# Kernel tuning notes

Measured on AMD Instinct MI355X. Metric: run time of the kernel, lower is better.

The kernel has to match this reference:

```python
import jax, jax.numpy as jnp
import numpy as np

B, T, N = 128, 1024, 64


def setup_inputs() -> dict:
    key = jax.random.key(0)
    k1, k2, k3, k4, k5 = jax.random.split(key, 5)
    potentials = jax.random.normal(k1, (B, T, N), dtype=jnp.float32)
    tags = jax.random.randint(k2, (B, T), 0, N, dtype=jnp.int32)
    # valid lengths in [T//2, T] so every sequence has at least one step
    sequence_length = jax.random.randint(k3, (B,), T // 2, T + 1, dtype=jnp.int32)
    chain_kernel = jax.random.normal(k4, (N, N), dtype=jnp.float32)
    sample_weight = jax.random.uniform(k5, (B,), dtype=jnp.float32)
    return {
        "potentials": potentials,
        "tags": tags,
        "sequence_length": sequence_length,
        "chain_kernel": chain_kernel,
        "sample_weight": sample_weight,
    }


def _crf_sequence_score(potentials, tags, sequence_length, chain_kernel):
    # potentials: [B,T,N], tags: [B,T] int, chain_kernel: [N,N]
    Bx, Tx, Nx = potentials.shape
    t_idx = jnp.arange(Tx)
    mask = (t_idx[None, :] < sequence_length[:, None]).astype(potentials.dtype)  # [B,T]
    # unary score: potentials at the gold tag per step
    unary = jnp.take_along_axis(potentials, tags[..., None].astype(jnp.int32), axis=2)[..., 0]  # [B,T]
    unary_score = jnp.sum(unary * mask, axis=1)  # [B]
    # binary score: transitions tag[t] -> tag[t+1], valid if t+1 < seq_len
    trans_sc = chain_kernel[tags[:, :-1], tags[:, 1:]]  # [B,T-1]
    binary_score = jnp.sum(trans_sc * mask[:, 1:], axis=1)  # [B]
    return unary_score + binary_score


def _crf_log_norm(potentials, sequence_length, chain_kernel):
    # forward algorithm with lax.scan over time
    Bx, Tx, Nx = potentials.shape
    alpha0 = potentials[:, 0]  # [B,N]
    pots_rest = jnp.transpose(potentials[:, 1:], (1, 0, 2))  # [T-1,B,N]
    step_mask = (jnp.arange(1, Tx)[:, None] < sequence_length[None, :])  # [T-1,B]

    def step(alpha, inp):
        pot_t, m_t = inp  # [B,N], [B]
        # logsumexp over previous tag: alpha[b,i] + trans[i,j]
        new = jax.nn.logsumexp(alpha[:, :, None] + chain_kernel[None], axis=1) + pot_t
        alpha = jnp.where(m_t[:, None], new, alpha)
        return alpha, None

    alpha_T, _ = jax.lax.scan(step, alpha0, (pots_rest, step_mask))
    return jax.nn.logsumexp(alpha_T, axis=1)  # [B]


def reference(potentials, tags, sequence_length, chain_kernel, sample_weight):
    seq_score = _crf_sequence_score(potentials, tags, sequence_length, chain_kernel)
    log_norm = _crf_log_norm(potentials, sequence_length, chain_kernel)
    log_likelihood = seq_score - log_norm  # [B]
    crf_loss = -log_likelihood * sample_weight
    return jnp.mean(crf_loss)
```

## Files before the change

kernel.cpp:

```cpp
#include <hip/hip_runtime.h>
#include <math.h>

#define BB 128
#define TT 1024
#define NN 64
#define NCH 16
#define SCH 64

typedef __attribute__((ext_vector_type(4))) float f32x4;
typedef __attribute__((ext_vector_type(4))) short bf16x4;

__device__ __forceinline__ float wave_sum64(float v) {
#pragma unroll
  for (int o = 32; o > 0; o >>= 1) v += __shfl_xor(v, o, 64);
  return v;
}

__device__ __forceinline__ unsigned pkbf(float lo, float hi) {
  unsigned a = __float_as_uint(lo) + 0x8000u;
  unsigned b = __float_as_uint(hi) + 0x8000u;
  return __builtin_amdgcn_perm(b, a, 0x07060302u);
}

__device__ __forceinline__ int fexp(float x) {
  unsigned u = __float_as_uint(x);
  int e = (int)((u >> 23) & 0xffu) - 127;
  if ((u & 0x7f800000u) == 0) e = 0;
  return e;
}

__global__ __launch_bounds__(64, 4) void crf_phase1(
    const float* __restrict__ pot, const int* __restrict__ tags,
    const int* __restrict__ seqlen, const float* __restrict__ K,
    unsigned* __restrict__ Hg, int* __restrict__ Eexp, float* __restrict__ score,
    float* __restrict__ accf, unsigned* __restrict__ cnt) {
  __shared__ __align__(16) float ring[4 * 64];
  __shared__ __align__(16) unsigned sht[544];
  const int lane = threadIdx.x;
  const int blk = blockIdx.x;

  if (blk == 0 && lane == 0) { *accf = 0.0f; *cnt = 0u; }

  if (blk < BB) {
    const int b = blk;
    const int L = seqlen[b];
    const int* tg = tags + b * TT;
    const float* pbase = pot + (size_t)b * TT * NN;
    float acc = 0.0f;
    for (int t = lane; t < TT; t += 64) {
      if (t < L) {
        int cc = tg[t];
        float u = pbase[(size_t)t * 64 + cc];
        float tr = (t >= 1) ? K[tg[t - 1] * 64 + cc] : 0.0f;
        acc += u + tr;
      }
    }
    acc = wave_sum64(acc);
    if (lane == 0) score[b] = acc;
    return;
  }

  const int idx = blk - BB;
  const int c = idx >> 9;
  const int b = (idx >> 2) & (BB - 1);
  const int g = idx & 3;
  const int L = seqlen[b];
  const int q = lane >> 4, lm = lane & 15;
  const int rb = q * 4;

  const int t0 = c * SCH + 1;
  const int tend = (L < TT) ? L : TT;
  int nsteps = tend - t0;
  if (nsteps > SCH) nsteps = SCH;

  unsigned* Hc = Hg + (size_t)(b * NCH + c) * 2048 + g * 8 * 64;
  if (nsteps <= 0) {
#pragma unroll
    for (int w = 0; w < 8; w++) {
      int c0 = g * 16 + 2 * w;
      unsigned v = (lane == c0 ? 0x3F80u : 0u) | (lane == c0 + 1 ? 0x3F800000u : 0u);
      Hc[w * 64 + lane] = v;
    }
    if (lane == 0) Eexp[(b * NCH + c) * 4 + g] = 0;
    return;
  }

  bf16x4 Af[4][4];
#pragma unroll
  for (int mt = 0; mt < 4; mt++)
#pragma unroll
    for (int kt = 0; kt < 4; kt++) {
      float v0 = __expf(K[(kt * 16 + rb + 0) * 64 + mt * 16 + lm]);
      float v1 = __expf(K[(kt * 16 + rb + 1) * 64 + mt * 16 + lm]);
      float v2 = __expf(K[(kt * 16 + rb + 2) * 64 + mt * 16 + lm]);
      float v3 = __expf(K[(kt * 16 + rb + 3) * 64 + mt * 16 + lm]);
      uint2 u; u.x = pkbf(v0, v1); u.y = pkbf(v2, v3);
      Af[mt][kt] = *(bf16x4*)&u;
    }

  f32x4 D[4];
#pragma unroll
  for (int mt = 0; mt < 4; mt++) {
    f32x4 d;
#pragma unroll
    for (int r = 0; r < 4; r++)
      d[r] = __expf(K[(g * 16 + lm) * 64 + mt * 16 + rb + r]);
    D[mt] = d;
  }

  const float* Pj = pot + (size_t)b * TT * NN + lane;
#pragma unroll
  for (int k = 0; k < 3; k++) {
    int tt = t0 + k; tt = tt > TT - 1 ? TT - 1 : tt;
    ring[k * 64 + lane] = __expf(Pj[(size_t)tt * NN]);
  }
  int t3 = t0 + 3 > TT - 1 ? TT - 1 : t0 + 3;
  int t4 = t0 + 4 > TT - 1 ? TT - 1 : t0 + 4;
  float rawq0 = Pj[(size_t)t3 * NN];
  float rawq1 = Pj[(size_t)t4 * NN];

  f32x4 pxc[4], pxn[4];
#pragma unroll
  for (int kt = 0; kt < 4; kt++)
    pxc[kt] = *(const f32x4*)&ring[0 * 64 + kt * 16 + rb];

  int etot = 0;
#pragma unroll 2
  for (int s = 0; s < nsteps - 1; s++) {
    if ((s & 7) == 7) {
      float d00 = __int_as_float(__builtin_amdgcn_readfirstlane(__float_as_int(D[0][0])));
      int e = fexp(d00);
      float psc = ldexpf(1.0f, -e);
      etot += e;
#pragma unroll
      for (int kt = 0; kt < 4; kt++) pxc[kt] *= psc;
    }
    bf16x4 Bf[4];
#pragma unroll
    for (int kt = 0; kt < 4; kt++) {
      f32x4 pr = D[kt] * pxc[kt];
      uint2 u;
      u.x = pkbf(pr[0], pr[1]);
      u.y = pkbf(pr[2], pr[3]);
      Bf[kt] = *(bf16x4*)&u;
    }
#pragma unroll
    for (int kt = 0; kt < 4; kt++)
      pxn[kt] = *(const f32x4*)&ring[((s + 1) & 3) * 64 + kt * 16 + rb];
    ring[((s + 3) & 3) * 64 + lane] = __expf(rawq0);
    rawq0 = rawq1;
    {
      int tn = t0 + s + 5; tn = tn > TT - 1 ? TT - 1 : tn;
      rawq1 = Pj[(size_t)tn * NN];
    }
#pragma unroll
    for (int mt = 0; mt < 4; mt++) {
      f32x4 acc = {0.f, 0.f, 0.f, 0.f};
#pragma unroll
      for (int kt = 0; kt < 4; kt++)
        acc = __builtin_amdgcn_mfma_f32_16x16x16bf16_1k(Af[mt][kt], Bf[kt], acc, 0, 0, 0);
      D[mt] = acc;
    }
#pragma unroll
    for (int kt = 0; kt < 4; kt++) pxc[kt] = pxn[kt];
  }

  {
    float hf = __int_as_float(
        __builtin_amdgcn_readfirstlane(__float_as_int(D[0][0] * pxc[0][0])));
    int ef = fexp(hf);
    float sc = ldexpf(1.0f, -ef);
    etot += ef;
#pragma unroll
    for (int mt = 0; mt < 4; mt++) {
      f32x4 d = D[mt]; f32x4 pv = pxc[mt];
      int base = lm * 33 + mt * 8 + q * 2;
      sht[base]     = pkbf(d[0] * pv[0] * sc, d[1] * pv[1] * sc);
      sht[base + 1] = pkbf(d[2] * pv[2] * sc, d[3] * pv[3] * sc);
    }
#pragma unroll
    for (int w = 0; w < 8; w++) {
      unsigned short a0 = ((const unsigned short*)(sht + (2 * w) * 33 + (lane >> 1)))[lane & 1];
      unsigned short a1 = ((const unsigned short*)(sht + (2 * w + 1) * 33 + (lane >> 1)))[lane & 1];
      Hc[w * 64 + lane] = (unsigned)a0 | ((unsigned)a1 << 16);
    }
    if (lane == 0) Eexp[(b * NCH + c) * 4 + g] = etot;
  }
}

__global__ __launch_bounds__(64, 4) void crf_phase2(
    const float* __restrict__ pot, const unsigned* __restrict__ Hg,
    const int* __restrict__ Eexp, const float* __restrict__ score,
    const float* __restrict__ wgt, float* __restrict__ accf,
    unsigned* __restrict__ cnt, float* __restrict__ out) {
  __shared__ __align__(16) float sha[64];
  const int j = threadIdx.x;
  const int b = blockIdx.x;

  float a = __expf(pot[(size_t)b * TT * NN + j]);
  sha[j] = a;
  int atot = 0;

  const unsigned* Hb = Hg + (size_t)b * NCH * 2048;
  unsigned bufA[32], bufB[32];
#pragma unroll
  for (int k = 0; k < 32; k++) bufA[k] = Hb[k * 64 + j];
#pragma unroll
  for (int k = 0; k < 32; k++) bufB[k] = Hb[2048 + k * 64 + j];

#pragma unroll
  for (int cc = 0; cc < NCH; cc += 2) {
#pragma unroll
    for (int half = 0; half < 2; half++) {
      const int c = cc + half;
      unsigned* cur = half ? bufB : bufA;
      float S[4] = {0.f, 0.f, 0.f, 0.f};
#pragma unroll
      for (int w4 = 0; w4 < 16; w4++) {
        f32x4 av = *(const f32x4*)&sha[w4 * 4];
        unsigned r0 = cur[2 * w4], r1 = cur[2 * w4 + 1];
        S[w4 >> 2] += __uint_as_float(r0 << 16) * av[0] +
                      __uint_as_float(r0 & 0xffff0000u) * av[1] +
                      __uint_as_float(r1 << 16) * av[2] +
                      __uint_as_float(r1 & 0xffff0000u) * av[3];
      }
      const int eb = b * 64 + c * 4;
      int e0 = Eexp[eb + 0], e1 = Eexp[eb + 1], e2 = Eexp[eb + 2], e3 = Eexp[eb + 3];
      int em = max(max(e0, e1), max(e2, e3));
      float Sc = ldexpf(S[0], e0 - em) + ldexpf(S[1], e1 - em) +
                 ldexpf(S[2], e2 - em) + ldexpf(S[3], e3 - em);
      int er = fexp(__int_as_float(
          __builtin_amdgcn_readfirstlane(__float_as_int(Sc))));
      a = ldexpf(Sc, -er);
      atot += em + er;
      sha[j] = a;
      if (c + 2 < NCH) {
        const unsigned* Hn = Hb + (size_t)(c + 2) * 2048;
#pragma unroll
        for (int k = 0; k < 32; k++) cur[k] = Hn[k * 64 + j];
      }
    }
  }

  float ssum = wave_sum64(a);
  if (j == 0) {
    float lognorm = __logf(ssum) + (float)atot * 0.69314718055994530942f;
    float loss = -(score[b] - lognorm) * wgt[b];
    atomicAdd(accf, loss * (1.0f / BB));
    __threadfence();
    unsigned old = atomicAdd(cnt, 1u);
    if (old == BB - 1) out[0] = atomicAdd(accf, 0.0f);
  }
}

__global__ __launch_bounds__(64) void crf_main_fb(
    const float* __restrict__ pot, const int* __restrict__ tags,
    const int* __restrict__ seqlen, const float* __restrict__ K,
    float* __restrict__ ws) {
  __shared__ float sh[4096];
  const int lane = threadIdx.x;
  const int blk = blockIdx.x;
  if (blk < BB) {
    const int b = blk;
    const int L = seqlen[b];
    float Ec[64];
#pragma unroll
    for (int i = 0; i < 64; i++) Ec[i] = __expf(K[i * 64 + lane]);
    const float* pb = pot + (size_t)b * TT * NN + lane;
    float av = __expf(pb[0]);
    int etot = 0;
    sh[lane] = av;
    float pf[8];
#pragma unroll
    for (int k = 0; k < 8; k++) pf[k] = pb[(size_t)(1 + k) * 64];
    for (int t0 = 1; t0 < L; t0 += 8) {
#pragma unroll
      for (int k = 0; k < 8; k++) {
        const int t = t0 + k;
        const float pe = __expf(pf[k]);
        int tn = t + 8; tn = tn > (TT - 1) ? (TT - 1) : tn;
        pf[k] = pb[(size_t)tn * 64];
        const float4* arow = (const float4*)(sh + ((t - 1) & 1) * 64);
        float s[8];
#pragma unroll
        for (int qq = 0; qq < 8; qq++) s[qq] = 0.0f;
#pragma unroll
        for (int qq = 0; qq < 16; qq++) {
          float4 a4 = arow[qq];
          float pr = fmaf(a4.x, Ec[4 * qq + 0], fmaf(a4.y, Ec[4 * qq + 1],
                     fmaf(a4.z, Ec[4 * qq + 2], a4.w * Ec[4 * qq + 3])));
          s[qq & 7] += pr;
        }
        float S = ((s[0] + s[1]) + (s[2] + s[3])) + ((s[4] + s[5]) + (s[6] + s[7]));
        if (t < L) {
          av = S * pe;
          if ((t & 3) == 0) {
            float m0 = __shfl(av, 0, 64);
            int e = ((__float_as_int(m0) >> 23) & 0xff) - 126;
            av = ldexpf(av, -e);
            etot += e;
          }
        }
        sh[(t & 1) * 64 + lane] = av;
      }
    }
    float ssum = wave_sum64(av);
    if (lane == 0) ws[b] = __logf(ssum) + (float)etot * 0.69314718055994530942f;
  } else {
    const int b = blk - BB;
    const int L = seqlen[b];
    for (int i = lane; i < 4096; i += 64) sh[i] = K[i];
    __syncthreads();
    const int* tg = tags + b * TT;
    const float* pbase = pot + (size_t)b * TT * NN;
    float acc = 0.0f;
    for (int t = lane; t < TT; t += 64) {
      if (t < L) {
        int cc = tg[t];
        float u = pbase[(size_t)t * 64 + cc];
        float tr = 0.0f;
        if (t >= 1) tr = sh[tg[t - 1] * 64 + cc];
        acc += u + tr;
      }
    }
    acc = wave_sum64(acc);
    if (lane == 0) ws[BB + b] = acc;
  }
}

__global__ __launch_bounds__(128) void crf_combine_fb(
    const float* __restrict__ ws, const float* __restrict__ wgt,
    float* __restrict__ out) {
  const int i = threadIdx.x;
  float lv = -(ws[BB + i] - ws[i]) * wgt[i];
  lv = wave_sum64(lv);
  __shared__ float p[2];
  if ((i & 63) == 0) p[i >> 6] = lv;
  __syncthreads();
  if (i == 0) out[0] = (p[0] + p[1]) * (1.0f / 128.0f);
}

extern "C" void kernel_launch(void* const* d_in, const int* in_sizes, int n_in,
                              void* d_out, int out_size, void* d_ws, size_t ws_size,
                              hipStream_t stream) {
  const float* pot    = (const float*)d_in[0];
  const int*   tags   = (const int*)d_in[1];
  const int*   seqlen = (const int*)d_in[2];
  const float* K      = (const float*)d_in[3];
  const float* wgt    = (const float*)d_in[4];

  const size_t HG_DW = (size_t)BB * NCH * 2048;
  const size_t NEXP  = (size_t)BB * NCH * 4;
  const size_t need  = (HG_DW + NEXP + BB + 2) * 4;

  if (ws_size >= need) {
    unsigned* Hg    = (unsigned*)d_ws;
    int* Eexp       = (int*)(Hg + HG_DW);
    float* score    = (float*)(Eexp + NEXP);
    float* accf     = score + BB;
    unsigned* cntp  = (unsigned*)(accf + 1);
    crf_phase1<<<BB + BB * NCH * 4, 64, 0, stream>>>(pot, tags, seqlen, K, Hg, Eexp,
                                                     score, accf, cntp);
    crf_phase2<<<BB, 64, 0, stream>>>(pot, Hg, Eexp, score, wgt, accf, cntp,
                                      (float*)d_out);
  } else {
    float* ws = (float*)d_ws;
    crf_main_fb<<<256, 64, 0, stream>>>(pot, tags, seqlen, K, ws);
    crf_combine_fb<<<1, 128, 0, stream>>>(ws, wgt, (float*)d_out);
  }
}
```

Before: 170.2 us.

## Pack four waves per block in phase1 and split phase2 chunk combine across waves

Phase1 now runs four independent wavefronts per 256-thread block, each with its own LDS ring and staging buffer, which cuts the block count by four. Phase2 goes from one wave to four waves per batch row. Each wave handles one 16-row slice of the chunk matrix, broadcasts alpha by shuffle instead of through LDS, and joins partial sums through a double-buffered shared array with a block barrier per chunk. This spreads the serial phase2 chain and its register buffers over more lanes, at the cost of sixteen __syncthreads per row and more shuffles.

```diff
diff --git a/kernel.cpp b/kernel.cpp
--- a/kernel.cpp
+++ b/kernel.cpp
@@ -29,20 +29,21 @@
   return e;
 }
 
-__global__ __launch_bounds__(64, 4) void crf_phase1(
+__global__ __launch_bounds__(256, 6) void crf_phase1(
     const float* __restrict__ pot, const int* __restrict__ tags,
     const int* __restrict__ seqlen, const float* __restrict__ K,
     unsigned* __restrict__ Hg, int* __restrict__ Eexp, float* __restrict__ score,
     float* __restrict__ accf, unsigned* __restrict__ cnt) {
-  __shared__ __align__(16) float ring[4 * 64];
-  __shared__ __align__(16) unsigned sht[544];
-  const int lane = threadIdx.x;
-  const int blk = blockIdx.x;
-
-  if (blk == 0 && lane == 0) { *accf = 0.0f; *cnt = 0u; }
-
-  if (blk < BB) {
-    const int b = blk;
+  __shared__ __align__(16) float ring[4][4 * 64];
+  __shared__ __align__(16) unsigned sht[4][544];
+  const int wv = threadIdx.x >> 6;
+  const int lane = threadIdx.x & 63;
+  const int tid = blockIdx.x * 4 + wv;
+
+  if (blockIdx.x == 0 && threadIdx.x == 0) { *accf = 0.0f; *cnt = 0u; }
+
+  if (tid < BB) {
+    const int b = tid;
     const int L = seqlen[b];
     const int* tg = tags + b * TT;
     const float* pbase = pot + (size_t)b * TT * NN;
@@ -60,7 +61,10 @@
     return;
   }
 
-  const int idx = blk - BB;
+  float* const rg = ring[wv];
+  unsigned* const shp = sht[wv];
+
+  const int idx = tid - BB;
   const int c = idx >> 9;
   const int b = (idx >> 2) & (BB - 1);
   const int g = idx & 3;
@@ -112,7 +116,7 @@
 #pragma unroll
   for (int k = 0; k < 3; k++) {
     int tt = t0 + k; tt = tt > TT - 1 ? TT - 1 : tt;
-    ring[k * 64 + lane] = __expf(Pj[(size_t)tt * NN]);
+    rg[k * 64 + lane] = __expf(Pj[(size_t)tt * NN]);
   }
   int t3 = t0 + 3 > TT - 1 ? TT - 1 : t0 + 3;
   int t4 = t0 + 4 > TT - 1 ? TT - 1 : t0 + 4;
@@ -122,7 +126,7 @@
   f32x4 pxc[4], pxn[4];
 #pragma unroll
   for (int kt = 0; kt < 4; kt++)
-    pxc[kt] = *(const f32x4*)&ring[0 * 64 + kt * 16 + rb];
+    pxc[kt] = *(const f32x4*)&rg[0 * 64 + kt * 16 + rb];
 
   int etot = 0;
 #pragma unroll 2
@@ -146,8 +150,8 @@
     }
 #pragma unroll
     for (int kt = 0; kt < 4; kt++)
-      pxn[kt] = *(const f32x4*)&ring[((s + 1) & 3) * 64 + kt * 16 + rb];
-    ring[((s + 3) & 3) * 64 + lane] = __expf(rawq0);
+      pxn[kt] = *(const f32x4*)&rg[((s + 1) & 3) * 64 + kt * 16 + rb];
+    rg[((s + 3) & 3) * 64 + lane] = __expf(rawq0);
     rawq0 = rawq1;
     {
       int tn = t0 + s + 5; tn = tn > TT - 1 ? TT - 1 : tn;
@@ -175,75 +179,81 @@
     for (int mt = 0; mt < 4; mt++) {
       f32x4 d = D[mt]; f32x4 pv = pxc[mt];
       int base = lm * 33 + mt * 8 + q * 2;
-      sht[base]     = pkbf(d[0] * pv[0] * sc, d[1] * pv[1] * sc);
-      sht[base + 1] = pkbf(d[2] * pv[2] * sc, d[3] * pv[3] * sc);
+      shp[base]     = pkbf(d[0] * pv[0] * sc, d[1] * pv[1] * sc);
+      shp[base + 1] = pkbf(d[2] * pv[2] * sc, d[3] * pv[3] * sc);
     }
 #pragma unroll
     for (int w = 0; w < 8; w++) {
-      unsigned short a0 = ((const unsigned short*)(sht + (2 * w) * 33 + (lane >> 1)))[lane & 1];
-      unsigned short a1 = ((const unsigned short*)(sht + (2 * w + 1) * 33 + (lane >> 1)))[lane & 1];
+      unsigned short a0 = ((const unsigned short*)(shp + (2 * w) * 33 + (lane >> 1)))[lane & 1];
+      unsigned short a1 = ((const unsigned short*)(shp + (2 * w + 1) * 33 + (lane >> 1)))[lane & 1];
       Hc[w * 64 + lane] = (unsigned)a0 | ((unsigned)a1 << 16);
     }
     if (lane == 0) Eexp[(b * NCH + c) * 4 + g] = etot;
   }
 }
 
-__global__ __launch_bounds__(64, 4) void crf_phase2(
+__global__ __launch_bounds__(256, 4) void crf_phase2(
     const float* __restrict__ pot, const unsigned* __restrict__ Hg,
     const int* __restrict__ Eexp, const float* __restrict__ score,
     const float* __restrict__ wgt, float* __restrict__ accf,
     unsigned* __restrict__ cnt, float* __restrict__ out) {
-  __shared__ __align__(16) float sha[64];
-  const int j = threadIdx.x;
+  __shared__ __align__(16) float sp[2][4 * 64];
+  const int g = threadIdx.x >> 6;
+  const int j = threadIdx.x & 63;
   const int b = blockIdx.x;
 
   float a = __expf(pot[(size_t)b * TT * NN + j]);
-  sha[j] = a;
   int atot = 0;
-
-  const unsigned* Hb = Hg + (size_t)b * NCH * 2048;
-  unsigned bufA[32], bufB[32];
-#pragma unroll
-  for (int k = 0; k < 32; k++) bufA[k] = Hb[k * 64 + j];
-#pragma unroll
-  for (int k = 0; k < 32; k++) bufB[k] = Hb[2048 + k * 64 + j];
-
-#pragma unroll
-  for (int cc = 0; cc < NCH; cc += 2) {
-#pragma unroll
-    for (int half = 0; half < 2; half++) {
-      const int c = cc + half;
-      unsigned* cur = half ? bufB : bufA;
-      float S[4] = {0.f, 0.f, 0.f, 0.f};
-#pragma unroll
-      for (int w4 = 0; w4 < 16; w4++) {
-        f32x4 av = *(const f32x4*)&sha[w4 * 4];
-        unsigned r0 = cur[2 * w4], r1 = cur[2 * w4 + 1];
-        S[w4 >> 2] += __uint_as_float(r0 << 16) * av[0] +
-                      __uint_as_float(r0 & 0xffff0000u) * av[1] +
-                      __uint_as_float(r1 << 16) * av[2] +
-                      __uint_as_float(r1 & 0xffff0000u) * av[3];
-      }
-      const int eb = b * 64 + c * 4;
-      int e0 = Eexp[eb + 0], e1 = Eexp[eb + 1], e2 = Eexp[eb + 2], e3 = Eexp[eb + 3];
-      int em = max(max(e0, e1), max(e2, e3));
-      float Sc = ldexpf(S[0], e0 - em) + ldexpf(S[1], e1 - em) +
-                 ldexpf(S[2], e2 - em) + ldexpf(S[3], e3 - em);
-      int er = fexp(__int_as_float(
-          __builtin_amdgcn_readfirstlane(__float_as_int(Sc))));
-      a = ldexpf(Sc, -er);
-      atot += em + er;
-      sha[j] = a;
-      if (c + 2 < NCH) {
-        const unsigned* Hn = Hb + (size_t)(c + 2) * 2048;
-#pragma unroll
-        for (int k = 0; k < 32; k++) cur[k] = Hn[k * 64 + j];
-      }
-    }
-  }
+  const int ee = Eexp[b * 64 + j];
+
+  const unsigned* Hb = Hg + (size_t)b * NCH * 2048 + g * 8 * 64;
+  unsigned u0[8], u1[8];
+#pragma unroll
+  for (int w = 0; w < 8; w++) u0[w] = Hb[w * 64 + j];
+#pragma unroll
+  for (int w = 0; w < 8; w++) u1[w] = Hb[2048 + w * 64 + j];
+
+#define CHUNK(cur, c)                                                          \
+  do {                                                                         \
+    float S = 0.0f;                                                            \
+    _Pragma("unroll")                                                          \
+    for (int w = 0; w < 8; w++) {                                              \
+      float a0 = __shfl(a, 16 * g + 2 * w, 64);                                \
+      float a1 = __shfl(a, 16 * g + 2 * w + 1, 64);                            \
+      unsigned r = cur[w];                                                     \
+      S += __uint_as_float(r << 16) * a0 +                                     \
+           __uint_as_float(r & 0xffff0000u) * a1;                              \
+    }                                                                          \
+    sp[(c) & 1][g * 64 + j] = S;                                               \
+    if ((c) + 2 < NCH) {   \
+      const unsigned* Hn = Hb + (size_t)((c) + 2) * 2048;                      \
+      _Pragma("unroll")                                                        \
+      for (int w = 0; w < 8; w++) cur[w] = Hn[w * 64 + j];                     \
+    }                                                                          \
+    __syncthreads();                                                           \
+    int e0 = __shfl(ee, (c) * 4 + 0, 64);                                      \
+    int e1 = __shfl(ee, (c) * 4 + 1, 64);                                      \
+    int e2 = __shfl(ee, (c) * 4 + 2, 64);                                      \
+    int e3 = __shfl(ee, (c) * 4 + 3, 64);                                      \
+    int em = max(max(e0, e1), max(e2, e3));                                    \
+    float Sc = ldexpf(sp[(c) & 1][0 * 64 + j], e0 - em) +                      \
+               ldexpf(sp[(c) & 1][1 * 64 + j], e1 - em) +                      \
+               ldexpf(sp[(c) & 1][2 * 64 + j], e2 - em) +                      \
+               ldexpf(sp[(c) & 1][3 * 64 + j], e3 - em);                       \
+    int er = fexp(__int_as_float(                                              \
+        __builtin_amdgcn_readfirstlane(__float_as_int(Sc))));                  \
+    a = ldexpf(Sc, -er);                                                       \
+    atot += em + er;                                                           \
+  } while (0)
+
+  CHUNK(u0, 0);  CHUNK(u1, 1);  CHUNK(u0, 2);  CHUNK(u1, 3);
+  CHUNK(u0, 4);  CHUNK(u1, 5);  CHUNK(u0, 6);  CHUNK(u1, 7);
+  CHUNK(u0, 8);  CHUNK(u1, 9);  CHUNK(u0, 10); CHUNK(u1, 11);
+  CHUNK(u0, 12); CHUNK(u1, 13); CHUNK(u0, 14); CHUNK(u1, 15);
+#undef CHUNK
 
   float ssum = wave_sum64(a);
-  if (j == 0) {
+  if (threadIdx.x == 0) {
     float lognorm = __logf(ssum) + (float)atot * 0.69314718055994530942f;
     float loss = -(score[b] - lognorm) * wgt[b];
     atomicAdd(accf, loss * (1.0f / BB));
@@ -359,10 +369,11 @@
     float* score    = (float*)(Eexp + NEXP);
     float* accf     = score + BB;
     unsigned* cntp  = (unsigned*)(accf + 1);
-    crf_phase1<<<BB + BB * NCH * 4, 64, 0, stream>>>(pot, tags, seqlen, K, Hg, Eexp,
-                                                     score, accf, cntp);
-    crf_phase2<<<BB, 64, 0, stream>>>(pot, Hg, Eexp, score, wgt, accf, cntp,
-                                      (float*)d_out);
+    crf_phase1<<<(BB + BB * NCH * 4) / 4, 256, 0, stream>>>(pot, tags, seqlen, K,
+                                                            Hg, Eexp, score, accf,
+                                                            cntp);
+    crf_phase2<<<BB, 256, 0, stream>>>(pot, Hg, Eexp, score, wgt, accf, cntp,
+                                       (float*)d_out);
   } else {
     float* ws = (float*)d_ws;
     crf_main_fb<<<256, 64, 0, stream>>>(pot, tags, seqlen, K, ws);
```

Result: slower. 192.3 us (+13.0%).
